# Kernel tuning notes

Measured on AMD Instinct MI355X. Metric: run time of the kernel, lower is better.

The kernel has to match this reference:

```python
import jax, jax.numpy as jnp
import numpy as np

H = 512
B = 128
S = 512


def setup_inputs() -> dict:
    key = jax.random.key(0)
    ks = jax.random.split(key, 12)
    s = 1.0 / np.sqrt(H)
    return {
        "input": jax.random.normal(ks[0], (B, H), jnp.float32),
        "h": jax.random.normal(ks[1], (B, H), jnp.float32),
        "c": jax.random.normal(ks[2], (B, H), jnp.float32),
        "enc_outputs": jax.random.normal(ks[3], (B, S, H), jnp.float32),
        "mask": jnp.ones((B, S), jnp.float32),
        # attention params
        "W1": jax.random.uniform(ks[4], (H, H), jnp.float32, -s, s),
        "W2": jax.random.uniform(ks[5], (H, H), jnp.float32, -s, s),
        "b2": jax.random.uniform(ks[6], (H,), jnp.float32, -s, s),
        "V": jax.random.uniform(ks[7], (H, 1), jnp.float32, -s, s),
        # LSTMCell params (torch gate order: i, f, g, o)
        "W_ih": jax.random.uniform(ks[8], (4 * H, H), jnp.float32, -s, s),
        "W_hh": jax.random.uniform(ks[9], (4 * H, H), jnp.float32, -s, s),
        "b_ih": jax.random.uniform(ks[10], (4 * H,), jnp.float32, -s, s),
        "b_hh": jax.random.uniform(ks[11], (4 * H,), jnp.float32, -s, s),
    }


def _lstm_cell(x, h, c, W_ih, W_hh, b_ih, b_hh):
    gates = x @ W_ih.T + b_ih + h @ W_hh.T + b_hh  # [B, 4H]
    i, f, g, o = jnp.split(gates, 4, axis=1)
    i = jax.nn.sigmoid(i)
    f = jax.nn.sigmoid(f)
    g = jnp.tanh(g)
    o = jax.nn.sigmoid(o)
    c_new = f * c + i * g
    h_new = o * jnp.tanh(c_new)
    return h_new, c_new


def reference(input, h, c, enc_outputs, mask, W1, W2, b2, V, W_ih, W_hh, b_ih, b_hh):
    h_new, c_new = _lstm_cell(input, h, c, W_ih, W_hh, b_ih, b_hh)
    # Bahdanau additive attention
    w1e = jnp.einsum("bsh,oh->bso", enc_outputs, W1)          # [B,S,H]
    w2h = (h_new @ W2.T + b2)[:, None, :]                      # [B,1,H]
    u = jnp.tanh(w1e + w2h)                                    # [B,S,H]
    a = jnp.einsum("bsh,h->bs", u, V[:, 0])                    # [B,S]
    a = 10.0 * jnp.tanh(a)
    policy = jax.nn.softmax(a + jnp.log(mask), axis=1)         # [B,S]
    return policy, h_new, c_new
```

## Files before the change

kernel.cpp:

```cpp
#include <hip/hip_runtime.h>
#include <hip/hip_bf16.h>
#include <math.h>

typedef __bf16 bf16;
typedef __bf16 bf16x4 __attribute__((ext_vector_type(4)));
typedef __bf16 bf16x8 __attribute__((ext_vector_type(8)));
typedef float  f32x4  __attribute__((ext_vector_type(4)));

#define HD 512
#define NB 128
#define NS 512
#define MS (NB*NS)

__device__ __forceinline__ float sigmoidf_(float x){ return 1.0f/(1.0f+expf(-x)); }

__device__ __forceinline__ float fast_tanh(float x){
    float ax = fabsf(x);
    float e  = __expf(-2.0f*ax);
    float t  = (1.0f - e) * __builtin_amdgcn_rcpf(1.0f + e);
    return copysignf(t, x);
}

__global__ __launch_bounds__(256) void cvt_w1_frag(const float* __restrict__ W1, bf16* __restrict__ W1s){
    int F = blockIdx.x*4 + (threadIdx.x>>6);
    int l = threadIdx.x & 63;
    int fnl = F & 3, ki = (F>>2) & 15, g = F>>6;
    int row = (g*4 + fnl)*16 + (l & 15);
    int kk  = ki*32 + (l >> 4)*8;
    const f32x4* gp = (const f32x4*)&W1[(size_t)row*512 + kk];
    f32x4 v0 = gp[0], v1 = gp[1];
    bf16x8 hv;
    #pragma unroll
    for (int j=0;j<4;++j){ hv[j]=(bf16)v0[j]; hv[4+j]=(bf16)v1[j]; }
    *(bf16x8*)&W1s[(size_t)F*512 + (size_t)l*8] = hv;
}

__global__ __launch_bounds__(256) void gemm_split(
    const float* __restrict__ A1, const float* __restrict__ A2,
    const float* __restrict__ B1, const float* __restrict__ B2,
    const float* __restrict__ bias1, const float* __restrict__ bias2,
    float* __restrict__ C, int N, int ksize, int ldct)
{
    __shared__ bf16 Ah[64][32], Al[64][32], Bh[64][32], Bl[64][32];
    int tid = threadIdx.x;
    int bm = blockIdx.x, bn = blockIdx.y, ks = blockIdx.z;
    int kfrom = ks*ksize, kend = kfrom + ksize;
    float* Cz = C + (size_t)ks * N * ldct;
    int w = tid>>6, l = tid&63;
    int wm = w>>1, wn = w&1;
    f32x4 acc[2][2] = {};
    for (int k0 = kfrom; k0 < kend; k0 += 32){
        const float* Ap = (k0 < 512) ? A1 : A2;
        const float* Bp = (k0 < 512) ? B1 : B2;
        int kk = k0 & 511;
        __syncthreads();
        #pragma unroll
        for (int q = 0; q < 2; ++q){
            int id  = q*256 + tid;
            int row = id >> 3, c4 = (id & 7)*4;
            f32x4 va = *(const f32x4*)&Ap[(size_t)(bm*64+row)*512 + kk + c4];
            f32x4 vb = *(const f32x4*)&Bp[(size_t)(bn*64+row)*512 + kk + c4];
            bf16x4 vah, val_, vbh, vbl;
            #pragma unroll
            for (int j=0;j<4;++j){
                bf16 ha = (bf16)va[j]; vah[j]=ha; val_[j]=(bf16)(va[j]-(float)ha);
                bf16 hb = (bf16)vb[j]; vbh[j]=hb; vbl[j]=(bf16)(vb[j]-(float)hb);
            }
            *(bf16x4*)&Ah[row][c4] = vah;  *(bf16x4*)&Al[row][c4] = val_;
            *(bf16x4*)&Bh[row][c4] = vbh;  *(bf16x4*)&Bl[row][c4] = vbl;
        }
        __syncthreads();
        int koff = (l>>4)*8;
        int ar = wm*32 + (l&15);
        int br = wn*32 + (l&15);
        bf16x8 ah[2], al[2], bh[2], bl[2];
        ah[0]=*(const bf16x8*)&Ah[ar][koff];    ah[1]=*(const bf16x8*)&Ah[ar+16][koff];
        al[0]=*(const bf16x8*)&Al[ar][koff];    al[1]=*(const bf16x8*)&Al[ar+16][koff];
        bh[0]=*(const bf16x8*)&Bh[br][koff];    bh[1]=*(const bf16x8*)&Bh[br+16][koff];
        bl[0]=*(const bf16x8*)&Bl[br][koff];    bl[1]=*(const bf16x8*)&Bl[br+16][koff];
        #pragma unroll
        for (int fm=0; fm<2; ++fm)
        #pragma unroll
        for (int fn=0; fn<2; ++fn){
            acc[fm][fn] = __builtin_amdgcn_mfma_f32_16x16x32_bf16(ah[fm], bh[fn], acc[fm][fn],0,0,0);
            acc[fm][fn] = __builtin_amdgcn_mfma_f32_16x16x32_bf16(ah[fm], bl[fn], acc[fm][fn],0,0,0);
            acc[fm][fn] = __builtin_amdgcn_mfma_f32_16x16x32_bf16(al[fm], bh[fn], acc[fm][fn],0,0,0);
        }
    }
    #pragma unroll
    for (int fm=0; fm<2; ++fm)
    #pragma unroll
    for (int fn=0; fn<2; ++fn){
        #pragma unroll
        for (int r=0; r<4; ++r){
            int m = bm*64 + wm*32 + fm*16 + ((l>>4)<<2) + r;
            int n = bn*64 + wn*32 + fn*16 + (l&15);
            float v = acc[fm][fn][r];
            if (ks == 0){
                if (bias1) v += bias1[m];
                if (bias2) v += bias2[m];
            }
            Cz[(size_t)n*ldct + m] = v;
        }
    }
}

__global__ __launch_bounds__(256) void lstm_pointwise(
    const float* __restrict__ gatesT, const float* __restrict__ c_in,
    float* __restrict__ h_out, float* __restrict__ c_out)
{
    int t = blockIdx.x*256 + threadIdx.x;
    int b = t >> 9, hh = t & 511;
    const float* gp = gatesT + (size_t)b*2048 + hh;
    float gi=0.f, gf=0.f, gg=0.f, go=0.f;
    #pragma unroll
    for (int ks=0; ks<4; ++ks){
        const float* p = gp + (size_t)ks*262144;
        gi += p[0]; gf += p[512]; gg += p[1024]; go += p[1536];
    }
    float i = sigmoidf_(gi), f = sigmoidf_(gf), g = tanhf(gg), o = sigmoidf_(go);
    float cn = f*c_in[t] + i*g;
    float hn = o*tanhf(cn);
    h_out[t] = hn;  c_out[t] = cn;
}

__global__ __launch_bounds__(512,4) void attn_main(
    const float* __restrict__ enc, const bf16* __restrict__ W1s,
    const float* __restrict__ w2hp, const float* __restrict__ Vv,
    float* __restrict__ a_out)
{
    __shared__ bf16 Alds[64*512];
    __shared__ float w2h_s[512];
    __shared__ float V_s[512];
    __shared__ float red[64][8];
    const int tid = threadIdx.x, w = tid>>6, l = tid&63;
    const int lr = l & 15, lk = l >> 4;
    const int m0 = blockIdx.x * 64;
    const int bidx = blockIdx.x >> 3;
    w2h_s[tid] = w2hp[(size_t)bidx*512 + tid] + w2hp[(size_t)65536 + bidx*512 + tid];
    V_s[tid]   = Vv[tid];

    const bf16* Bbase = W1s + (size_t)w*32768 + (size_t)l*8;

    bf16x8 bA[4], bB[4];
    #pragma unroll
    for (int fn=0; fn<4; ++fn) bA[fn] = *(const bf16x8*)(Bbase + fn*512);

    #pragma unroll
    for (int it = 0; it < 8; ++it){
        int c   = it*512 + tid;
        int row = c >> 6, s = c & 63;
        const f32x4* gp = (const f32x4*)&enc[(size_t)(m0+row)*512 + s*8];
        f32x4 v0 = __builtin_nontemporal_load(gp);
        f32x4 v1 = __builtin_nontemporal_load(gp+1);
        bf16x8 hv;
        #pragma unroll
        for (int j=0;j<4;++j){ hv[j]=(bf16)v0[j]; hv[4+j]=(bf16)v1[j]; }
        int slot = s ^ (row & 15);
        *(bf16x8*)((char*)Alds + row*1024 + slot*16) = hv;
    }
    __syncthreads();

    f32x4 acc[4][4] = {};

    #pragma unroll
    for (int kp = 0; kp < 8; ++kp){
        int ki0 = 2*kp, ki1 = 2*kp+1;
        #pragma unroll
        for (int fn=0; fn<4; ++fn) bB[fn] = *(const bf16x8*)(Bbase + fn*512 + (size_t)ki1*2048);
        {
            bf16x8 af[4];
            #pragma unroll
            for (int fm=0; fm<4; ++fm){
                int row = fm*16 + lr;
                int slot = (ki0*4 + lk) ^ (row & 15);
                af[fm] = *(const bf16x8*)((const char*)Alds + row*1024 + slot*16);
            }
            #pragma unroll
            for (int fm=0; fm<4; ++fm)
            #pragma unroll
            for (int fn=0; fn<4; ++fn)
                acc[fm][fn] = __builtin_amdgcn_mfma_f32_16x16x32_bf16(af[fm], bA[fn], acc[fm][fn],0,0,0);
        }
        if (kp < 7){
            #pragma unroll
            for (int fn=0; fn<4; ++fn) bA[fn] = *(const bf16x8*)(Bbase + fn*512 + (size_t)(ki0+2)*2048);
        }
        {
            bf16x8 af[4];
            #pragma unroll
            for (int fm=0; fm<4; ++fm){
                int row = fm*16 + lr;
                int slot = (ki1*4 + lk) ^ (row & 15);
                af[fm] = *(const bf16x8*)((const char*)Alds + row*1024 + slot*16);
            }
            #pragma unroll
            for (int fm=0; fm<4; ++fm)
            #pragma unroll
            for (int fn=0; fn<4; ++fn)
                acc[fm][fn] = __builtin_amdgcn_mfma_f32_16x16x32_bf16(af[fm], bB[fn], acc[fm][fn],0,0,0);
        }
    }

    #pragma unroll
    for (int fm=0; fm<4; ++fm){
        float asum[4] = {0.f,0.f,0.f,0.f};
        #pragma unroll
        for (int fn=0; fn<4; ++fn){
            int o = w*64 + fn*16 + lr;
            float wv = w2h_s[o], vv = V_s[o];
            #pragma unroll
            for (int r=0;r<4;++r)
                asum[r] += fast_tanh(acc[fm][fn][r] + wv) * vv;
        }
        #pragma unroll
        for (int off=1; off<16; off<<=1){
            #pragma unroll
            for (int r=0;r<4;++r) asum[r] += __shfl_xor(asum[r], off, 64);
        }
        if (lr == 0){
            #pragma unroll
            for (int r=0;r<4;++r) red[fm*16 + lk*4 + r][w] = asum[r];
        }
    }
    __syncthreads();
    if (tid < 64){
        float a = 0.f;
        #pragma unroll
        for (int q=0;q<8;++q) a += red[tid][q];
        a_out[m0 + tid] = 10.0f * fast_tanh(a);
    }
}

__global__ __launch_bounds__(512) void softmax_k(
    const float* __restrict__ a10, const float* __restrict__ mask,
    float* __restrict__ out)
{
    int b = blockIdx.x, tid = threadIdx.x;
    __shared__ float sred[8];
    float v = a10[(size_t)b*512 + tid] + logf(mask[(size_t)b*512 + tid]);
    float m = v;
    #pragma unroll
    for (int off=1; off<64; off<<=1) m = fmaxf(m, __shfl_xor(m, off, 64));
    if ((tid&63)==0) sred[tid>>6] = m;
    __syncthreads();
    float mt = sred[0];
    #pragma unroll
    for (int i=1;i<8;++i) mt = fmaxf(mt, sred[i]);
    float e = expf(v - mt);
    float s = e;
    #pragma unroll
    for (int off=1; off<64; off<<=1) s += __shfl_xor(s, off, 64);
    __syncthreads();
    if ((tid&63)==0) sred[tid>>6] = s;
    __syncthreads();
    float st = 0.f;
    #pragma unroll
    for (int i=0;i<8;++i) st += sred[i];
    out[(size_t)b*512 + tid] = e / st;
}

extern "C" void kernel_launch(void* const* d_in, const int* in_sizes, int n_in,
                              void* d_out, int out_size, void* d_ws, size_t ws_size,
                              hipStream_t stream)
{
    const float* x    = (const float*)d_in[0];
    const float* h    = (const float*)d_in[1];
    const float* c    = (const float*)d_in[2];
    const float* enc  = (const float*)d_in[3];
    const float* mask = (const float*)d_in[4];
    const float* W1   = (const float*)d_in[5];
    const float* W2   = (const float*)d_in[6];
    const float* b2   = (const float*)d_in[7];
    const float* V    = (const float*)d_in[8];
    const float* Wih  = (const float*)d_in[9];
    const float* Whh  = (const float*)d_in[10];
    const float* bih  = (const float*)d_in[11];
    const float* bhh  = (const float*)d_in[12];

    float* out_policy = (float*)d_out;
    float* out_h = out_policy + MS;
    float* out_c = out_policy + 2*MS;

    float* ws_f   = (float*)d_ws;
    float* gatesT = ws_f;
    float* w2hp   = ws_f + 1048576;
    float* a10    = ws_f + 1179648;
    bf16*  W1s    = (bf16*)(ws_f + 1245184);

    cvt_w1_frag<<<128, 256, 0, stream>>>(W1, W1s);
    gemm_split<<<dim3(32,2,4), 256, 0, stream>>>(Wih, Whh, x, h, bih, bhh, gatesT, 128, 256, 2048);
    lstm_pointwise<<<256, 256, 0, stream>>>(gatesT, c, out_h, out_c);
    gemm_split<<<dim3(8,2,2), 256, 0, stream>>>(W2, nullptr, out_h, nullptr, b2, nullptr, w2hp, 128, 256, 512);
    attn_main<<<1024, 512, 0, stream>>>(enc, W1s, w2hp, V, a10);
    softmax_k<<<128, 512, 0, stream>>>(a10, mask, out_policy);
}
```

Before: 98.27 us.

## Stage W1 fragments through double-buffered LDS via direct global-to-LDS DMA

```diff
diff --git a/kernel.cpp b/kernel.cpp
--- a/kernel.cpp
+++ b/kernel.cpp
@@ -21,10 +21,16 @@
     return copysignf(t, x);
 }
 
+__device__ __forceinline__ void dma16(const void* g, void* l){
+    __builtin_amdgcn_global_load_lds(
+        (const __attribute__((address_space(1))) unsigned int*)g,
+        (__attribute__((address_space(3))) unsigned int*)l, 16, 0, 0);
+}
+
 __global__ __launch_bounds__(256) void cvt_w1_frag(const float* __restrict__ W1, bf16* __restrict__ W1s){
     int F = blockIdx.x*4 + (threadIdx.x>>6);
     int l = threadIdx.x & 63;
-    int fnl = F & 3, ki = (F>>2) & 15, g = F>>6;
+    int fnl = F & 3, g = (F>>2) & 7, ki = F>>5;
     int row = (g*4 + fnl)*16 + (l & 15);
     int kk  = ki*32 + (l >> 4)*8;
     const f32x4* gp = (const f32x4*)&W1[(size_t)row*512 + kk];
@@ -124,12 +130,13 @@
     h_out[t] = hn;  c_out[t] = cn;
 }
 
-__global__ __launch_bounds__(512,4) void attn_main(
+__global__ __launch_bounds__(512,2) void attn_main(
     const float* __restrict__ enc, const bf16* __restrict__ W1s,
     const float* __restrict__ w2hp, const float* __restrict__ Vv,
     float* __restrict__ a_out)
 {
     __shared__ bf16 Alds[64*512];
+    __shared__ bf16 Bbuf[2][16384];
     __shared__ float w2h_s[512];
     __shared__ float V_s[512];
     __shared__ float red[64][8];
@@ -140,19 +147,20 @@
     w2h_s[tid] = w2hp[(size_t)bidx*512 + tid] + w2hp[(size_t)65536 + bidx*512 + tid];
     V_s[tid]   = Vv[tid];
 
-    const bf16* Bbase = W1s + (size_t)w*32768 + (size_t)l*8;
-
-    bf16x8 bA[4], bB[4];
-    #pragma unroll
-    for (int fn=0; fn<4; ++fn) bA[fn] = *(const bf16x8*)(Bbase + fn*512);
+#define B_DMA(KI, BUF) { \
+    _Pragma("unroll") \
+    for (int j=0; j<4; ++j) \
+        dma16(W1s + (size_t)(KI)*16384 + (j*8+w)*512 + l*8, \
+              &Bbuf[BUF][(j*8+w)*512]); }
+
+    B_DMA(0, 0)
 
     #pragma unroll
     for (int it = 0; it < 8; ++it){
         int c   = it*512 + tid;
         int row = c >> 6, s = c & 63;
         const f32x4* gp = (const f32x4*)&enc[(size_t)(m0+row)*512 + s*8];
-        f32x4 v0 = __builtin_nontemporal_load(gp);
-        f32x4 v1 = __builtin_nontemporal_load(gp+1);
+        f32x4 v0 = gp[0], v1 = gp[1];
         bf16x8 hv;
         #pragma unroll
         for (int j=0;j<4;++j){ hv[j]=(bf16)v0[j]; hv[4+j]=(bf16)v1[j]; }
@@ -164,43 +172,28 @@
     f32x4 acc[4][4] = {};
 
     #pragma unroll
-    for (int kp = 0; kp < 8; ++kp){
-        int ki0 = 2*kp, ki1 = 2*kp+1;
-        #pragma unroll
-        for (int fn=0; fn<4; ++fn) bB[fn] = *(const bf16x8*)(Bbase + fn*512 + (size_t)ki1*2048);
-        {
-            bf16x8 af[4];
-            #pragma unroll
-            for (int fm=0; fm<4; ++fm){
-                int row = fm*16 + lr;
-                int slot = (ki0*4 + lk) ^ (row & 15);
-                af[fm] = *(const bf16x8*)((const char*)Alds + row*1024 + slot*16);
-            }
-            #pragma unroll
-            for (int fm=0; fm<4; ++fm)
-            #pragma unroll
-            for (int fn=0; fn<4; ++fn)
-                acc[fm][fn] = __builtin_amdgcn_mfma_f32_16x16x32_bf16(af[fm], bA[fn], acc[fm][fn],0,0,0);
-        }
-        if (kp < 7){
-            #pragma unroll
-            for (int fn=0; fn<4; ++fn) bA[fn] = *(const bf16x8*)(Bbase + fn*512 + (size_t)(ki0+2)*2048);
-        }
-        {
-            bf16x8 af[4];
-            #pragma unroll
-            for (int fm=0; fm<4; ++fm){
-                int row = fm*16 + lr;
-                int slot = (ki1*4 + lk) ^ (row & 15);
-                af[fm] = *(const bf16x8*)((const char*)Alds + row*1024 + slot*16);
-            }
-            #pragma unroll
-            for (int fm=0; fm<4; ++fm)
-            #pragma unroll
-            for (int fn=0; fn<4; ++fn)
-                acc[fm][fn] = __builtin_amdgcn_mfma_f32_16x16x32_bf16(af[fm], bB[fn], acc[fm][fn],0,0,0);
-        }
-    }
+    for (int ki = 0; ki < 16; ++ki){
+        const int cur = ki & 1;
+        if (ki < 15) B_DMA(ki+1, cur^1)
+        bf16x8 af[4];
+        #pragma unroll
+        for (int fm=0; fm<4; ++fm){
+            int row = fm*16 + lr;
+            int slot = (ki*4 + lk) ^ (row & 15);
+            af[fm] = *(const bf16x8*)((const char*)Alds + row*1024 + slot*16);
+        }
+        bf16x8 bf[4];
+        #pragma unroll
+        for (int fn=0; fn<4; ++fn)
+            bf[fn] = *(const bf16x8*)((const char*)&Bbuf[cur][0] + (w*4+fn)*1024 + l*16);
+        #pragma unroll
+        for (int fm=0; fm<4; ++fm)
+        #pragma unroll
+        for (int fn=0; fn<4; ++fn)
+            acc[fm][fn] = __builtin_amdgcn_mfma_f32_16x16x32_bf16(af[fm], bf[fn], acc[fm][fn],0,0,0);
+        __syncthreads();
+    }
+#undef B_DMA
 
     #pragma unroll
     for (int fm=0; fm<4; ++fm){
```

After: 119.1 us. +21.2%, slower.
